# Optimization experiments

Measured on AMD Instinct MI355X. Metric: run time of the kernel, lower is better.

The kernel has to match this reference:

```python
import jax, jax.numpy as jnp
import numpy as np

NUM_HEADS = 16
GROUP_NUM = 4
HIDDEN = 1024
HEAD_DIM = HIDDEN // NUM_HEADS
EPS = 1e-5


def layernorm(x, g, b):
    mu = jnp.mean(x, axis=-1, keepdims=True)
    var = jnp.var(x, axis=-1, keepdims=True)
    return (x - mu) * jax.lax.rsqrt(var + EPS) * g + b


def setup_inputs() -> dict:
    key = jax.random.key(0)
    ks = jax.random.split(key, 12)
    s = 0.02
    return {
        "hidden_state": jax.random.normal(ks[0], (2, 2048, HIDDEN), jnp.float32),
        "wq": jax.random.normal(ks[1], (HIDDEN, HIDDEN), jnp.float32) * s,
        "bq": jnp.zeros((HIDDEN,), jnp.float32),
        "wk": jax.random.normal(ks[2], (GROUP_NUM * HEAD_DIM, HIDDEN), jnp.float32) * s,
        "bk": jnp.zeros((GROUP_NUM * HEAD_DIM,), jnp.float32),
        "wv": jax.random.normal(ks[3], (GROUP_NUM * HEAD_DIM, HIDDEN), jnp.float32) * s,
        "bv": jnp.zeros((GROUP_NUM * HEAD_DIM,), jnp.float32),
        "wo": jax.random.normal(ks[4], (HIDDEN, HIDDEN), jnp.float32) * s,
        "bo": jnp.zeros((HIDDEN,), jnp.float32),
        "ln_g": jnp.ones((HIDDEN,), jnp.float32),
        "ln_b": jnp.zeros((HIDDEN,), jnp.float32),
        "w1": jax.random.normal(ks[5], (HIDDEN, HIDDEN), jnp.float32) * s,
        "b1": jnp.zeros((HIDDEN,), jnp.float32),
        "w2": jax.random.normal(ks[6], (HIDDEN, HIDDEN), jnp.float32) * s,
        "b2": jnp.zeros((HIDDEN,), jnp.float32),
        "fln_g": jnp.ones((HIDDEN,), jnp.float32),
        "fln_b": jnp.zeros((HIDDEN,), jnp.float32),
    }


def reference(hidden_state, wq, bq, wk, bk, wv, bv, wo, bo, ln_g, ln_b,
              w1, b1, w2, b2, fln_g, fln_b):
    B, S, H = hidden_state.shape
    hpg = NUM_HEADS // GROUP_NUM  # heads per KV group

    q = hidden_state @ wq.T + bq  # [B,S,H]
    k = hidden_state @ wk.T + bk  # [B,S,G*D]
    v = hidden_state @ wv.T + bv

    q = q.reshape(B, S, NUM_HEADS, HEAD_DIM).transpose(0, 2, 1, 3)      # [B,Hh,S,D]
    k = k.reshape(B, S, GROUP_NUM, HEAD_DIM).transpose(0, 2, 1, 3)      # [B,G,S,D]
    v = v.reshape(B, S, GROUP_NUM, HEAD_DIM).transpose(0, 2, 1, 3)
    # expand KV groups to full head count (consecutive repeat, matching torch expand+reshape)
    k = jnp.repeat(k, hpg, axis=1)  # [B,Hh,S,D]
    v = jnp.repeat(v, hpg, axis=1)

    scale = 1.0 / jnp.sqrt(jnp.float32(HEAD_DIM))
    scores = jnp.einsum('bhsd,bhtd->bhst', q, k) * scale  # [B,Hh,S,S]
    probs = jax.nn.softmax(scores, axis=-1)
    attn = jnp.einsum('bhst,bhtd->bhsd', probs, v)  # [B,Hh,S,D]

    # Faithful to source: transpose(-1,-2) then raw flat view to [B, S, Hh*D]
    attn = jnp.swapaxes(attn, -1, -2).reshape(B, -1, HEAD_DIM * NUM_HEADS)

    out = layernorm(hidden_state + attn @ wo.T + bo, ln_g, ln_b)
    ffn = out @ w1.T + b1
    ffn = jax.nn.relu(ffn) @ w2.T + b2
    return layernorm(out + ffn, fln_g, fln_b)
```

## Files before the change

### kernel.cpp

```cpp
#include <hip/hip_runtime.h>
#include <math.h>

#define HIDDEN 1024
#define SEQ 2048

typedef __attribute__((ext_vector_type(8))) short short8;
typedef __attribute__((ext_vector_type(4))) float f32x4;

__device__ __forceinline__ unsigned short f2bf(float x) {
  union { float f; unsigned u; } c; c.f = x;
  unsigned r = c.u + 0x7FFFu + ((c.u >> 16) & 1u);
  return (unsigned short)(r >> 16);
}
__device__ __forceinline__ float bf2f(unsigned short h) {
  union { unsigned u; float f; } c; c.u = ((unsigned)h) << 16;
  return c.f;
}

__device__ __forceinline__ void async_copy16(const void* g, void* l) {
  __builtin_amdgcn_global_load_lds(
      (const __attribute__((address_space(1))) unsigned int*)g,
      (__attribute__((address_space(3))) unsigned int*)l, 16, 0, 0);
}

__global__ __launch_bounds__(256) void cvt_all(
    const float* __restrict__ hs, const float* __restrict__ wq,
    const float* __restrict__ wk, const float* __restrict__ wv,
    const float* __restrict__ wo, const float* __restrict__ w1,
    const float* __restrict__ w2,
    unsigned short* __restrict__ hsb, unsigned short* __restrict__ wqb,
    unsigned short* __restrict__ wkb, unsigned short* __restrict__ wvb,
    unsigned short* __restrict__ wob, unsigned short* __restrict__ w1b,
    unsigned short* __restrict__ w2b)
{
  const int i = blockIdx.x * 256 + threadIdx.x;
  const float* src; unsigned short* dst; int off;
  if (i < 1048576)      { src = hs; dst = hsb; off = i; }
  else if (i < 1310720) { src = wq; dst = wqb; off = i - 1048576; }
  else if (i < 1376256) { src = wk; dst = wkb; off = i - 1310720; }
  else if (i < 1441792) { src = wv; dst = wvb; off = i - 1376256; }
  else if (i < 1703936) { src = wo; dst = wob; off = i - 1441792; }
  else if (i < 1966080) { src = w1; dst = w1b; off = i - 1703936; }
  else                  { src = w2; dst = w2b; off = i - 1966080; }
  float4 v = ((const float4*)src)[off];
  ushort4 o;
  o.x = f2bf(v.x); o.y = f2bf(v.y); o.z = f2bf(v.z); o.w = f2bf(v.w);
  ((ushort4*)dst)[off] = o;
}

template<bool RELU>
__global__ __launch_bounds__(256) void gemm_mfma(
    const unsigned short* __restrict__ A, const unsigned short* __restrict__ W,
    const float* __restrict__ bias, unsigned short* __restrict__ C,
    int M, int N, int K)
{
  __shared__ unsigned short As[64 * 64];
  __shared__ unsigned short Bs[64 * 64];
  const int tid = threadIdx.x;
  const int lane = tid & 63, wave = tid >> 6;
  const int ln = lane & 15, quad = lane >> 4;
  const int wm = (wave >> 1) * 32, wn = (wave & 1) * 32;
  const int m0 = blockIdx.y * 64, n0 = blockIdx.x * 64;

  f32x4 acc[2][2];
#pragma unroll
  for (int i = 0; i < 2; ++i)
#pragma unroll
    for (int j = 0; j < 2; ++j) acc[i][j] = (f32x4){0.f, 0.f, 0.f, 0.f};

  for (int k0 = 0; k0 < K; k0 += 64) {
#pragma unroll
    for (int it = 0; it < 2; ++it) {
      const int c = (wave * 2 + it) * 64 + lane;
      const int row = c >> 3, gc = (c & 7) ^ (row & 7);
      async_copy16(A + (size_t)(m0 + row) * K + k0 + gc * 8,
                   &As[(wave * 2 + it) * 512]);
      async_copy16(W + (size_t)(n0 + row) * K + k0 + gc * 8,
                   &Bs[(wave * 2 + it) * 512]);
    }
    __syncthreads();

    short8 af[2][2], bfr[2][2];
#pragma unroll
    for (int i = 0; i < 2; ++i) {
      const int row = wm + i * 16 + ln;
#pragma unroll
      for (int f = 0; f < 2; ++f) {
        const int ch = row * 8 + ((f * 4 + quad) ^ (row & 7));
        af[i][f] = *(const short8*)&As[ch * 8];
      }
    }
#pragma unroll
    for (int j = 0; j < 2; ++j) {
      const int row = wn + j * 16 + ln;
#pragma unroll
      for (int f = 0; f < 2; ++f) {
        const int ch = row * 8 + ((f * 4 + quad) ^ (row & 7));
        bfr[j][f] = *(const short8*)&Bs[ch * 8];
      }
    }
#pragma unroll
    for (int i = 0; i < 2; ++i)
#pragma unroll
      for (int j = 0; j < 2; ++j) {
        acc[i][j] = __builtin_amdgcn_mfma_f32_16x16x32_bf16(af[i][0], bfr[j][0], acc[i][j], 0, 0, 0);
        acc[i][j] = __builtin_amdgcn_mfma_f32_16x16x32_bf16(af[i][1], bfr[j][1], acc[i][j], 0, 0, 0);
      }
    __syncthreads();
  }

#pragma unroll
  for (int j = 0; j < 2; ++j) {
    const int n = n0 + wn + j * 16 + ln;
    const float bv = bias[n];
#pragma unroll
    for (int i = 0; i < 2; ++i) {
#pragma unroll
      for (int rr = 0; rr < 4; ++rr) {
        const int m = m0 + wm + i * 16 + quad * 4 + rr;
        float v = acc[i][j][rr] + bv;
        if (RELU) v = fmaxf(v, 0.f);
        C[(size_t)m * N + n] = f2bf(v);
      }
    }
  }
}

__global__ __launch_bounds__(256) void gemm_qkv(
    const unsigned short* __restrict__ A,
    const unsigned short* __restrict__ Wq, const unsigned short* __restrict__ Wk,
    const unsigned short* __restrict__ Wv,
    const float* __restrict__ bq, const float* __restrict__ bk,
    const float* __restrict__ bv,
    unsigned short* __restrict__ Qo, unsigned short* __restrict__ Ko,
    unsigned short* __restrict__ Vt)
{
  __shared__ unsigned short As[64 * 64];
  __shared__ unsigned short Bs[128 * 64];
  const int bx = blockIdx.x;
  int mode, nw0;
  const unsigned short* W;
  const float* bias;
  if (bx < 8)       { mode = 0; W = Wq; bias = bq; nw0 = bx * 128; }
  else if (bx < 10) { mode = 1; W = Wk; bias = bk; nw0 = (bx - 8) * 128; }
  else              { mode = 2; W = Wv; bias = bv; nw0 = (bx - 10) * 128; }

  const int tid = threadIdx.x;
  const int lane = tid & 63, wave = tid >> 6;
  const int ln = lane & 15, quad = lane >> 4;
  const int wm = (wave >> 1) * 32, wn = (wave & 1) * 64;
  const int m0 = blockIdx.y * 64;
  const int K = 1024;

  f32x4 acc[2][4];
#pragma unroll
  for (int i = 0; i < 2; ++i)
#pragma unroll
    for (int j = 0; j < 4; ++j) acc[i][j] = (f32x4){0.f, 0.f, 0.f, 0.f};

  for (int k0 = 0; k0 < K; k0 += 64) {
#pragma unroll
    for (int it = 0; it < 2; ++it) {
      const int c = (wave * 2 + it) * 64 + lane;
      const int row = c >> 3, gc = (c & 7) ^ (row & 7);
      async_copy16(A + (size_t)(m0 + row) * K + k0 + gc * 8,
                   &As[(wave * 2 + it) * 512]);
    }
#pragma unroll
    for (int it = 0; it < 4; ++it) {
      const int c = (wave * 4 + it) * 64 + lane;
      const int row = c >> 3, gc = (c & 7) ^ (row & 7);
      async_copy16(W + (size_t)(nw0 + row) * K + k0 + gc * 8,
                   &Bs[(wave * 4 + it) * 512]);
    }
    __syncthreads();

    short8 af[2][2], bfr[4][2];
#pragma unroll
    for (int i = 0; i < 2; ++i) {
      const int row = wm + i * 16 + ln;
#pragma unroll
      for (int f = 0; f < 2; ++f) {
        const int ch = row * 8 + ((f * 4 + quad) ^ (row & 7));
        af[i][f] = *(const short8*)&As[ch * 8];
      }
    }
#pragma unroll
    for (int j = 0; j < 4; ++j) {
      const int row = wn + j * 16 + ln;
#pragma unroll
      for (int f = 0; f < 2; ++f) {
        const int ch = row * 8 + ((f * 4 + quad) ^ (row & 7));
        bfr[j][f] = *(const short8*)&Bs[ch * 8];
      }
    }
#pragma unroll
    for (int i = 0; i < 2; ++i)
#pragma unroll
      for (int j = 0; j < 4; ++j) {
        acc[i][j] = __builtin_amdgcn_mfma_f32_16x16x32_bf16(af[i][0], bfr[j][0], acc[i][j], 0, 0, 0);
        acc[i][j] = __builtin_amdgcn_mfma_f32_16x16x32_bf16(af[i][1], bfr[j][1], acc[i][j], 0, 0, 0);
      }
    __syncthreads();
  }

#pragma unroll
  for (int j = 0; j < 4; ++j) {
    const int nl = nw0 + wn + j * 16 + ln;
    const float bvv = bias[nl];
#pragma unroll
    for (int i = 0; i < 2; ++i) {
#pragma unroll
      for (int rr = 0; rr < 4; ++rr) {
        const int m = m0 + wm + i * 16 + quad * 4 + rr;
        const float v = acc[i][j][rr] + bvv;
        if (mode == 0) {
          Qo[(size_t)m * 1024 + nl] = f2bf(v);
        } else if (mode == 1) {
          Ko[(size_t)m * 256 + nl] = f2bf(v);
        } else {
          const int b = m >> 11, s = m & 2047;
          Vt[((size_t)b * 256 + nl) * SEQ + s] = f2bf(v);
        }
      }
    }
  }
}

__global__ __launch_bounds__(256) void attn_mfma(
    const unsigned short* __restrict__ Q, const unsigned short* __restrict__ Kb,
    const unsigned short* __restrict__ Vt, unsigned short* __restrict__ O)
{
  __shared__ unsigned short Ks[2][64 * 64];
  __shared__ unsigned short Vs[2][64 * 64];
  __shared__ unsigned short Ps[4 * 2 * 16 * 64];

  const int bid = blockIdx.x;
  const int qblk = bid & 15, h = (bid >> 4) & 15, b = bid >> 8, g = h >> 2;
  const int tid = threadIdx.x, lane = tid & 63, wave = tid >> 6;
  const int ln = lane & 15, quad = lane >> 4, q8 = quad * 8;
  const int s0 = qblk * 128;
  const float qscale = 0.125f * 1.44269504f;

  const int ln7 = ln & 7;
  const int x0 = (quad ^ ln7) * 8;
  const int x1 = ((4 + quad) ^ ln7) * 8;
  const int pswz = 2 * ln7;
  const int pbase = wave * 2048 + ln * 64;
  int pwr[4], prd[2];
#pragma unroll
  for (int jn = 0; jn < 4; ++jn) pwr[jn] = pbase + (((jn * 4 + quad) ^ pswz) << 2);
#pragma unroll
  for (int F = 0; F < 2; ++F)   prd[F] = pbase + (((8 * F + 2 * quad) ^ pswz) << 2);

  short8 ones;
#pragma unroll
  for (int e = 0; e < 8; ++e) ones[e] = (short)0x3F80;

  short8 qf[2][2];
#pragma unroll
  for (int qg = 0; qg < 2; ++qg) {
    const unsigned short* qsrc =
        Q + ((size_t)(b * SEQ + s0 + wave * 32 + qg * 16 + ln)) * 1024 + h * 64 + q8;
    qf[qg][0] = *(const short8*)qsrc;
    qf[qg][1] = *(const short8*)(qsrc + 32);
#pragma unroll
    for (int e = 0; e < 8; ++e) {
      qf[qg][0][e] = (short)f2bf(bf2f((unsigned short)qf[qg][0][e]) * qscale);
      qf[qg][1][e] = (short)f2bf(bf2f((unsigned short)qf[qg][1][e]) * qscale);
    }
  }

  const int srow = lane >> 3;
  const int sgcc = (lane & 7) ^ srow;

  auto stage = [&](int t0, int p) {
#pragma unroll
    for (int it = 0; it < 2; ++it) {
      const int row = wave * 16 + it * 8 + srow;
      async_copy16(Kb + (size_t)(b * SEQ + t0 + row) * 256 + g * 64 + sgcc * 8,
                   &Ks[p][(wave * 2 + it) * 512]);
      async_copy16(Vt + (size_t)(b * 256 + g * 64 + row) * SEQ + t0 + sgcc * 8,
                   &Vs[p][(wave * 2 + it) * 512]);
    }
  };

  f32x4 of[2][4];
  f32x4 ls[2];
#pragma unroll
  for (int qg = 0; qg < 2; ++qg) {
    ls[qg] = (f32x4){0.f, 0.f, 0.f, 0.f};
#pragma unroll
    for (int jd = 0; jd < 4; ++jd) of[qg][jd] = (f32x4){0.f, 0.f, 0.f, 0.f};
  }

  stage(0, 0);

  for (int t = 0; t < 32; ++t) {
    const int p = t & 1;
    if (t < 31) {
      stage((t + 1) * 64, p ^ 1);
      asm volatile("s_waitcnt vmcnt(4)" ::: "memory");
    } else {
      asm volatile("s_waitcnt vmcnt(0)" ::: "memory");
    }
    __builtin_amdgcn_s_barrier();
    asm volatile("" ::: "memory");

    f32x4 sc[2][4];
#pragma unroll
    for (int jn = 0; jn < 4; ++jn) {
      const int krow = (jn * 16 + ln) * 64;
      const short8 kf0 = *(const short8*)&Ks[p][krow + x0];
      const short8 kf1 = *(const short8*)&Ks[p][krow + x1];
#pragma unroll
      for (int qg = 0; qg < 2; ++qg) {
        f32x4 z = (f32x4){0.f, 0.f, 0.f, 0.f};
        z = __builtin_amdgcn_mfma_f32_16x16x32_bf16(kf0, qf[qg][0], z, 0, 0, 0);
        z = __builtin_amdgcn_mfma_f32_16x16x32_bf16(kf1, qf[qg][1], z, 0, 0, 0);
        sc[qg][jn] = z;
      }
    }

#pragma unroll
    for (int qg = 0; qg < 2; ++qg)
#pragma unroll
      for (int jn = 0; jn < 4; ++jn) {
        union { float f; unsigned u; } c0, c1, c2, c3;
        c0.f = exp2f(sc[qg][jn][0]);
        c1.f = exp2f(sc[qg][jn][1]);
        c2.f = exp2f(sc[qg][jn][2]);
        c3.f = exp2f(sc[qg][jn][3]);
        uint2 pk;
        pk.x = __builtin_amdgcn_perm(c1.u, c0.u, 0x07060302u);
        pk.y = __builtin_amdgcn_perm(c3.u, c2.u, 0x07060302u);
        *(uint2*)&Ps[qg * 1024 + pwr[jn]] = pk;
      }

    short8 pf[2][2];
#pragma unroll
    for (int qg = 0; qg < 2; ++qg) {
      pf[qg][0] = *(const short8*)&Ps[qg * 1024 + prd[0]];
      pf[qg][1] = *(const short8*)&Ps[qg * 1024 + prd[1]];
      ls[qg] = __builtin_amdgcn_mfma_f32_16x16x32_bf16(pf[qg][0], ones, ls[qg], 0, 0, 0);
      ls[qg] = __builtin_amdgcn_mfma_f32_16x16x32_bf16(pf[qg][1], ones, ls[qg], 0, 0, 0);
    }
#pragma unroll
    for (int jd = 0; jd < 4; ++jd) {
      const int vrow = (jd * 16 + ln) * 64;
      const short8 vf0 = *(const short8*)&Vs[p][vrow + x0];
      const short8 vf1 = *(const short8*)&Vs[p][vrow + x1];
#pragma unroll
      for (int qg = 0; qg < 2; ++qg) {
        of[qg][jd] = __builtin_amdgcn_mfma_f32_16x16x32_bf16(pf[qg][0], vf0, of[qg][jd], 0, 0, 0);
        of[qg][jd] = __builtin_amdgcn_mfma_f32_16x16x32_bf16(pf[qg][1], vf1, of[qg][jd], 0, 0, 0);
      }
    }

    asm volatile("" ::: "memory");
    __builtin_amdgcn_s_barrier();
    asm volatile("" ::: "memory");
  }

#pragma unroll
  for (int qg = 0; qg < 2; ++qg) {
    float inv[4];
#pragma unroll
    for (int r = 0; r < 4; ++r) inv[r] = 1.0f / ls[qg][r];
    const int sbase = s0 + wave * 32 + qg * 16 + quad * 4;
#pragma unroll
    for (int jd = 0; jd < 4; ++jd) {
      const int d = jd * 16 + ln;
      ushort4 ov;
      ov.x = f2bf(of[qg][jd][0] * inv[0]);
      ov.y = f2bf(of[qg][jd][1] * inv[1]);
      ov.z = f2bf(of[qg][jd][2] * inv[2]);
      ov.w = f2bf(of[qg][jd][3] * inv[3]);
      *(ushort4*)&O[((size_t)b * 1024 + h * 64 + d) * SEQ + sbase] = ov;
    }
  }
}

__device__ __forceinline__ void ln_core(float x[4], const float* gam, const float* bet,
                                        int tid, float out[4]) {
  float s1 = x[0] + x[1] + x[2] + x[3];
  float s2 = x[0] * x[0] + x[1] * x[1] + x[2] * x[2] + x[3] * x[3];
#pragma unroll
  for (int off = 1; off < 64; off <<= 1) {
    s1 += __shfl_xor(s1, off);
    s2 += __shfl_xor(s2, off);
  }
  __shared__ float r1[4], r2[4];
  const int wave = tid >> 6;
  if ((tid & 63) == 0) { r1[wave] = s1; r2[wave] = s2; }
  __syncthreads();
  s1 = r1[0] + r1[1] + r1[2] + r1[3];
  s2 = r2[0] + r2[1] + r2[2] + r2[3];
  const float mu  = s1 * (1.0f / HIDDEN);
  const float var = s2 * (1.0f / HIDDEN) - mu * mu;
  const float inv = rsqrtf(var + 1e-5f);
  float4 gv = *(const float4*)&gam[tid * 4];
  float4 bv = *(const float4*)&bet[tid * 4];
  out[0] = (x[0] - mu) * inv * gv.x + bv.x;
  out[1] = (x[1] - mu) * inv * gv.y + bv.y;
  out[2] = (x[2] - mu) * inv * gv.z + bv.z;
  out[3] = (x[3] - mu) * inv * gv.w + bv.w;
}

__global__ __launch_bounds__(256) void resid_ln1(
    const float* __restrict__ X, const unsigned short* __restrict__ Y,
    const float* __restrict__ gam, const float* __restrict__ bet,
    unsigned short* __restrict__ outb)
{
  const int row = blockIdx.x, tid = threadIdx.x;
  const size_t base = (size_t)row * HIDDEN + tid * 4;
  float4 a = *(const float4*)&X[base];
  ushort4 yv = *(const ushort4*)&Y[base];
  float x[4] = {a.x + bf2f(yv.x), a.y + bf2f(yv.y), a.z + bf2f(yv.z), a.w + bf2f(yv.w)};
  float o[4];
  ln_core(x, gam, bet, tid, o);
  ushort4 ov;
  ov.x = f2bf(o[0]); ov.y = f2bf(o[1]); ov.z = f2bf(o[2]); ov.w = f2bf(o[3]);
  *(ushort4*)&outb[base] = ov;
}

__global__ __launch_bounds__(256) void resid_ln2(
    const unsigned short* __restrict__ X, const unsigned short* __restrict__ Y,
    const float* __restrict__ gam, const float* __restrict__ bet,
    float* __restrict__ out)
{
  const int row = blockIdx.x, tid = threadIdx.x;
  const size_t base = (size_t)row * HIDDEN + tid * 4;
  ushort4 xv = *(const ushort4*)&X[base];
  ushort4 yv = *(const ushort4*)&Y[base];
  float x[4] = {bf2f(xv.x) + bf2f(yv.x), bf2f(xv.y) + bf2f(yv.y),
                bf2f(xv.z) + bf2f(yv.z), bf2f(xv.w) + bf2f(yv.w)};
  float o[4];
  ln_core(x, gam, bet, tid, o);
  float4 ov; ov.x = o[0]; ov.y = o[1]; ov.z = o[2]; ov.w = o[3];
  *(float4*)&out[base] = ov;
}

extern "C" void kernel_launch(void* const* d_in, const int* in_sizes, int n_in,
                              void* d_out, int out_size, void* d_ws, size_t ws_size,
                              hipStream_t stream)
{
  (void)in_sizes; (void)n_in; (void)out_size; (void)ws_size;
  const float* hs  = (const float*)d_in[0];
  const float* wq  = (const float*)d_in[1];
  const float* bq  = (const float*)d_in[2];
  const float* wk  = (const float*)d_in[3];
  const float* bk  = (const float*)d_in[4];
  const float* wv  = (const float*)d_in[5];
  const float* bvp = (const float*)d_in[6];
  const float* wo  = (const float*)d_in[7];
  const float* bo  = (const float*)d_in[8];
  const float* lng = (const float*)d_in[9];
  const float* lnb = (const float*)d_in[10];
  const float* w1  = (const float*)d_in[11];
  const float* b1  = (const float*)d_in[12];
  const float* w2  = (const float*)d_in[13];
  const float* b2  = (const float*)d_in[14];
  const float* flg = (const float*)d_in[15];
  const float* flb = (const float*)d_in[16];
  float* out = (float*)d_out;

  unsigned short* w = (unsigned short*)d_ws;
  unsigned short* wqb = w;
  unsigned short* wkb = w + 1048576;
  unsigned short* wvb = w + 1310720;
  unsigned short* wob = w + 1572864;
  unsigned short* w1b = w + 2621440;
  unsigned short* w2b = w + 3670016;
  unsigned short* hsb = w + 4718592;
  unsigned short* qb  = w + 8912896;
  unsigned short* kb  = w + 13107200;
  unsigned short* vt  = w + 14155776;
  unsigned short* att = w + 15204352;
  unsigned short* f1b = hsb;
  unsigned short* yb  = qb;
  unsigned short* obb = att;
  unsigned short* f2b = qb;

  dim3 blk(256);
  cvt_all<<<dim3(8704), blk, 0, stream>>>(hs, wq, wk, wv, wo, w1, w2,
                                          hsb, wqb, wkb, wvb, wob, w1b, w2b);

  gemm_qkv<<<dim3(12, 64), blk, 0, stream>>>(hsb, wqb, wkb, wvb, bq, bk, bvp,
                                             qb, kb, vt);
  attn_mfma<<<dim3(512), blk, 0, stream>>>(qb, kb, vt, att);
  gemm_mfma<false><<<dim3(16, 64), blk, 0, stream>>>(att, wob, bo, yb, 4096, 1024, 1024);
  resid_ln1<<<dim3(4096), blk, 0, stream>>>(hs, yb, lng, lnb, obb);
  gemm_mfma<true><<<dim3(16, 64), blk, 0, stream>>>(obb, w1b, b1, f1b, 4096, 1024, 1024);
  gemm_mfma<false><<<dim3(16, 64), blk, 0, stream>>>(f1b, w2b, b2, f2b, 4096, 1024, 1024);
  resid_ln2<<<dim3(4096), blk, 0, stream>>>(obb, f2b, flg, flb, out);
}
```

Baseline: 254.9 us.

## Double-buffer wider GEMM tiles and keep attention probabilities in registers

Result: faster. 242.4 us (-4.9%).

```diff
diff --git a/kernel.cpp b/kernel.cpp
--- a/kernel.cpp
+++ b/kernel.cpp
@@ -15,6 +15,20 @@
 __device__ __forceinline__ float bf2f(unsigned short h) {
   union { unsigned u; float f; } c; c.u = ((unsigned)h) << 16;
   return c.f;
+}
+
+__device__ __forceinline__ float fexp2(float x) {
+#if __has_builtin(__builtin_amdgcn_exp2f)
+  return __builtin_amdgcn_exp2f(x);
+#else
+  float r; asm("v_exp_f32 %0, %1" : "=v"(r) : "v"(x)); return r;
+#endif
+}
+
+__device__ __forceinline__ unsigned cvt_pk_bf16(float lo, float hi) {
+  unsigned r;
+  asm("v_cvt_pk_bf16_f32 %0, %1, %2" : "=v"(r) : "v"(lo), "v"(hi));
+  return r;
 }
 
 __device__ __forceinline__ void async_copy16(const void* g, void* l) {
@@ -49,68 +63,89 @@
 }
 
 template<bool RELU>
-__global__ __launch_bounds__(256) void gemm_mfma(
+__global__ __launch_bounds__(256) void gemm_wide(
     const unsigned short* __restrict__ A, const unsigned short* __restrict__ W,
     const float* __restrict__ bias, unsigned short* __restrict__ C,
     int M, int N, int K)
 {
-  __shared__ unsigned short As[64 * 64];
-  __shared__ unsigned short Bs[64 * 64];
+  __shared__ unsigned short As[2][64 * 64];
+  __shared__ unsigned short Bs[2][128 * 64];
   const int tid = threadIdx.x;
   const int lane = tid & 63, wave = tid >> 6;
   const int ln = lane & 15, quad = lane >> 4;
-  const int wm = (wave >> 1) * 32, wn = (wave & 1) * 32;
-  const int m0 = blockIdx.y * 64, n0 = blockIdx.x * 64;
-
-  f32x4 acc[2][2];
+  const int wm = (wave >> 1) * 32, wn = (wave & 1) * 64;
+  const int m0 = blockIdx.y * 64, n0 = blockIdx.x * 128;
+
+  f32x4 acc[2][4];
 #pragma unroll
   for (int i = 0; i < 2; ++i)
 #pragma unroll
-    for (int j = 0; j < 2; ++j) acc[i][j] = (f32x4){0.f, 0.f, 0.f, 0.f};
-
-  for (int k0 = 0; k0 < K; k0 += 64) {
+    for (int j = 0; j < 4; ++j) acc[i][j] = (f32x4){0.f, 0.f, 0.f, 0.f};
+
+  auto stage = [&](int k0, int p) {
 #pragma unroll
     for (int it = 0; it < 2; ++it) {
       const int c = (wave * 2 + it) * 64 + lane;
       const int row = c >> 3, gc = (c & 7) ^ (row & 7);
       async_copy16(A + (size_t)(m0 + row) * K + k0 + gc * 8,
-                   &As[(wave * 2 + it) * 512]);
+                   &As[p][(wave * 2 + it) * 512]);
+    }
+#pragma unroll
+    for (int it = 0; it < 4; ++it) {
+      const int c = (wave * 4 + it) * 64 + lane;
+      const int row = c >> 3, gc = (c & 7) ^ (row & 7);
       async_copy16(W + (size_t)(n0 + row) * K + k0 + gc * 8,
-                   &Bs[(wave * 2 + it) * 512]);
-    }
-    __syncthreads();
-
-    short8 af[2][2], bfr[2][2];
+                   &Bs[p][(wave * 4 + it) * 512]);
+    }
+  };
+
+  stage(0, 0);
+  const int NT = K >> 6;
+  for (int t = 0; t < NT; ++t) {
+    const int p = t & 1;
+    if (t < NT - 1) {
+      stage((t + 1) * 64, p ^ 1);
+      asm volatile("s_waitcnt vmcnt(6)" ::: "memory");
+    } else {
+      asm volatile("s_waitcnt vmcnt(0)" ::: "memory");
+    }
+    __builtin_amdgcn_s_barrier();
+    asm volatile("" ::: "memory");
+
+    short8 af[2][2], bfr[4][2];
 #pragma unroll
     for (int i = 0; i < 2; ++i) {
       const int row = wm + i * 16 + ln;
 #pragma unroll
       for (int f = 0; f < 2; ++f) {
         const int ch = row * 8 + ((f * 4 + quad) ^ (row & 7));
-        af[i][f] = *(const short8*)&As[ch * 8];
-      }
-    }
-#pragma unroll
-    for (int j = 0; j < 2; ++j) {
+        af[i][f] = *(const short8*)&As[p][ch * 8];
+      }
+    }
+#pragma unroll
+    for (int j = 0; j < 4; ++j) {
       const int row = wn + j * 16 + ln;
 #pragma unroll
       for (int f = 0; f < 2; ++f) {
         const int ch = row * 8 + ((f * 4 + quad) ^ (row & 7));
-        bfr[j][f] = *(const short8*)&Bs[ch * 8];
+        bfr[j][f] = *(const short8*)&Bs[p][ch * 8];
       }
     }
 #pragma unroll
     for (int i = 0; i < 2; ++i)
 #pragma unroll
-      for (int j = 0; j < 2; ++j) {
+      for (int j = 0; j < 4; ++j) {
         acc[i][j] = __builtin_amdgcn_mfma_f32_16x16x32_bf16(af[i][0], bfr[j][0], acc[i][j], 0, 0, 0);
         acc[i][j] = __builtin_amdgcn_mfma_f32_16x16x32_bf16(af[i][1], bfr[j][1], acc[i][j], 0, 0, 0);
       }
-    __syncthreads();
-  }
-
-#pragma unroll
-  for (int j = 0; j < 2; ++j) {
+
+    asm volatile("" ::: "memory");
+    __builtin_amdgcn_s_barrier();
+    asm volatile("" ::: "memory");
+  }
+
+#pragma unroll
+  for (int j = 0; j < 4; ++j) {
     const int n = n0 + wn + j * 16 + ln;
     const float bv = bias[n];
 #pragma unroll
@@ -233,7 +268,6 @@
 {
   __shared__ unsigned short Ks[2][64 * 64];
   __shared__ unsigned short Vs[2][64 * 64];
-  __shared__ unsigned short Ps[4 * 2 * 16 * 64];
 
   const int bid = blockIdx.x;
   const int qblk = bid & 15, h = (bid >> 4) & 15, b = bid >> 8, g = h >> 2;
@@ -245,13 +279,6 @@
   const int ln7 = ln & 7;
   const int x0 = (quad ^ ln7) * 8;
   const int x1 = ((4 + quad) ^ ln7) * 8;
-  const int pswz = 2 * ln7;
-  const int pbase = wave * 2048 + ln * 64;
-  int pwr[4], prd[2];
-#pragma unroll
-  for (int jn = 0; jn < 4; ++jn) pwr[jn] = pbase + (((jn * 4 + quad) ^ pswz) << 2);
-#pragma unroll
-  for (int F = 0; F < 2; ++F)   prd[F] = pbase + (((8 * F + 2 * quad) ^ pswz) << 2);
 
   short8 ones;
 #pragma unroll
@@ -278,7 +305,9 @@
 #pragma unroll
     for (int it = 0; it < 2; ++it) {
       const int row = wave * 16 + it * 8 + srow;
-      async_copy16(Kb + (size_t)(b * SEQ + t0 + row) * 256 + g * 64 + sgcc * 8,
+      const int skey = (row & 32) | ((row & 8) << 1) | ((row & 4) << 1) |
+                       ((row & 16) >> 2) | (row & 3);
+      async_copy16(Kb + (size_t)(b * SEQ + t0 + skey) * 256 + g * 64 + sgcc * 8,
                    &Ks[p][(wave * 2 + it) * 512]);
       async_copy16(Vt + (size_t)(b * 256 + g * 64 + row) * SEQ + t0 + sgcc * 8,
                    &Vs[p][(wave * 2 + it) * 512]);
@@ -322,29 +351,26 @@
       }
     }
 
-#pragma unroll
-    for (int qg = 0; qg < 2; ++qg)
-#pragma unroll
-      for (int jn = 0; jn < 4; ++jn) {
-        union { float f; unsigned u; } c0, c1, c2, c3;
-        c0.f = exp2f(sc[qg][jn][0]);
-        c1.f = exp2f(sc[qg][jn][1]);
-        c2.f = exp2f(sc[qg][jn][2]);
-        c3.f = exp2f(sc[qg][jn][3]);
-        uint2 pk;
-        pk.x = __builtin_amdgcn_perm(c1.u, c0.u, 0x07060302u);
-        pk.y = __builtin_amdgcn_perm(c3.u, c2.u, 0x07060302u);
-        *(uint2*)&Ps[qg * 1024 + pwr[jn]] = pk;
-      }
-
     short8 pf[2][2];
 #pragma unroll
     for (int qg = 0; qg < 2; ++qg) {
-      pf[qg][0] = *(const short8*)&Ps[qg * 1024 + prd[0]];
-      pf[qg][1] = *(const short8*)&Ps[qg * 1024 + prd[1]];
+#pragma unroll
+      for (int jn = 0; jn < 4; ++jn)
+#pragma unroll
+        for (int r = 0; r < 4; ++r) sc[qg][jn][r] = fexp2(sc[qg][jn][r]);
+#pragma unroll
+      for (int F = 0; F < 2; ++F) {
+        union { unsigned u[4]; short8 s; } pk;
+        pk.u[0] = cvt_pk_bf16(sc[qg][2 * F][0], sc[qg][2 * F][1]);
+        pk.u[1] = cvt_pk_bf16(sc[qg][2 * F][2], sc[qg][2 * F][3]);
+        pk.u[2] = cvt_pk_bf16(sc[qg][2 * F + 1][0], sc[qg][2 * F + 1][1]);
+        pk.u[3] = cvt_pk_bf16(sc[qg][2 * F + 1][2], sc[qg][2 * F + 1][3]);
+        pf[qg][F] = pk.s;
+      }
       ls[qg] = __builtin_amdgcn_mfma_f32_16x16x32_bf16(pf[qg][0], ones, ls[qg], 0, 0, 0);
       ls[qg] = __builtin_amdgcn_mfma_f32_16x16x32_bf16(pf[qg][1], ones, ls[qg], 0, 0, 0);
     }
+
 #pragma unroll
     for (int jd = 0; jd < 4; ++jd) {
       const int vrow = (jd * 16 + ln) * 64;
@@ -489,9 +515,9 @@
   gemm_qkv<<<dim3(12, 64), blk, 0, stream>>>(hsb, wqb, wkb, wvb, bq, bk, bvp,
                                              qb, kb, vt);
   attn_mfma<<<dim3(512), blk, 0, stream>>>(qb, kb, vt, att);
-  gemm_mfma<false><<<dim3(16, 64), blk, 0, stream>>>(att, wob, bo, yb, 4096, 1024, 1024);
+  gemm_wide<false><<<dim3(8, 64), blk, 0, stream>>>(att, wob, bo, yb, 4096, 1024, 1024);
   resid_ln1<<<dim3(4096), blk, 0, stream>>>(hs, yb, lng, lnb, obb);
-  gemm_mfma<true><<<dim3(16, 64), blk, 0, stream>>>(obb, w1b, b1, f1b, 4096, 1024, 1024);
-  gemm_mfma<false><<<dim3(16, 64), blk, 0, stream>>>(f1b, w2b, b2, f2b, 4096, 1024, 1024);
+  gemm_wide<true><<<dim3(8, 64), blk, 0, stream>>>(obb, w1b, b1, f1b, 4096, 1024, 1024);
+  gemm_wide<false><<<dim3(8, 64), blk, 0, stream>>>(f1b, w2b, b2, f2b, 4096, 1024, 1024);
   resid_ln2<<<dim3(4096), blk, 0, stream>>>(obb, f2b, flg, flb, out);
 }
```

## Keep attention probabilities in registers, enlarge query tiles, swizzle block order

Applied to the files above, without the earlier changes.

After: 244.1 us. 4.3% less time.

```diff
diff --git a/kernel.cpp b/kernel.cpp
--- a/kernel.cpp
+++ b/kernel.cpp
@@ -15,6 +15,16 @@
 __device__ __forceinline__ float bf2f(unsigned short h) {
   union { unsigned u; float f; } c; c.u = ((unsigned)h) << 16;
   return c.f;
+}
+
+__device__ __forceinline__ float fexp2(float x) {
+  float r; asm("v_exp_f32 %0, %1" : "=v"(r) : "v"(x)); return r;
+}
+
+__device__ __forceinline__ unsigned cvt_pk_bf16(float lo, float hi) {
+  unsigned r;
+  asm("v_cvt_pk_bf16_f32 %0, %1, %2" : "=v"(r) : "v"(lo), "v"(hi));
+  return r;
 }
 
 __device__ __forceinline__ void async_copy16(const void* g, void* l) {
@@ -60,7 +70,11 @@
   const int lane = tid & 63, wave = tid >> 6;
   const int ln = lane & 15, quad = lane >> 4;
   const int wm = (wave >> 1) * 32, wn = (wave & 1) * 32;
-  const int m0 = blockIdx.y * 64, n0 = blockIdx.x * 64;
+
+  const int flat = blockIdx.x;
+  const int swz = (flat & 7) * ((int)gridDim.x >> 3) + (flat >> 3);
+  const int ntx = N >> 6;
+  const int m0 = (swz / ntx) * 64, n0 = (swz % ntx) * 64;
 
   f32x4 acc[2][2];
 #pragma unroll
@@ -137,7 +151,11 @@
 {
   __shared__ unsigned short As[64 * 64];
   __shared__ unsigned short Bs[128 * 64];
-  const int bx = blockIdx.x;
+
+  const int flat = blockIdx.x;
+  const int swz = (flat & 7) * 96 + (flat >> 3);
+  const int bx = swz % 12, by = swz / 12;
+
   int mode, nw0;
   const unsigned short* W;
   const float* bias;
@@ -149,7 +167,7 @@
   const int lane = tid & 63, wave = tid >> 6;
   const int ln = lane & 15, quad = lane >> 4;
   const int wm = (wave >> 1) * 32, wn = (wave & 1) * 64;
-  const int m0 = blockIdx.y * 64;
+  const int m0 = by * 64;
   const int K = 1024;
 
   f32x4 acc[2][4];
@@ -233,35 +251,29 @@
 {
   __shared__ unsigned short Ks[2][64 * 64];
   __shared__ unsigned short Vs[2][64 * 64];
-  __shared__ unsigned short Ps[4 * 2 * 16 * 64];
-
-  const int bid = blockIdx.x;
-  const int qblk = bid & 15, h = (bid >> 4) & 15, b = bid >> 8, g = h >> 2;
+
+  const int hwb = blockIdx.x;
+  const int swz = (hwb & 7) * 32 + (hwb >> 3);
+  const int qblk = swz & 7, h = (swz >> 3) & 15, b = swz >> 7, g = h >> 2;
+
   const int tid = threadIdx.x, lane = tid & 63, wave = tid >> 6;
   const int ln = lane & 15, quad = lane >> 4, q8 = quad * 8;
-  const int s0 = qblk * 128;
+  const int s0 = qblk * 256;
   const float qscale = 0.125f * 1.44269504f;
 
   const int ln7 = ln & 7;
   const int x0 = (quad ^ ln7) * 8;
   const int x1 = ((4 + quad) ^ ln7) * 8;
-  const int pswz = 2 * ln7;
-  const int pbase = wave * 2048 + ln * 64;
-  int pwr[4], prd[2];
-#pragma unroll
-  for (int jn = 0; jn < 4; ++jn) pwr[jn] = pbase + (((jn * 4 + quad) ^ pswz) << 2);
-#pragma unroll
-  for (int F = 0; F < 2; ++F)   prd[F] = pbase + (((8 * F + 2 * quad) ^ pswz) << 2);
 
   short8 ones;
 #pragma unroll
   for (int e = 0; e < 8; ++e) ones[e] = (short)0x3F80;
 
-  short8 qf[2][2];
-#pragma unroll
-  for (int qg = 0; qg < 2; ++qg) {
+  short8 qf[4][2];
+#pragma unroll
+  for (int qg = 0; qg < 4; ++qg) {
     const unsigned short* qsrc =
-        Q + ((size_t)(b * SEQ + s0 + wave * 32 + qg * 16 + ln)) * 1024 + h * 64 + q8;
+        Q + ((size_t)(b * SEQ + s0 + wave * 64 + qg * 16 + ln)) * 1024 + h * 64 + q8;
     qf[qg][0] = *(const short8*)qsrc;
     qf[qg][1] = *(const short8*)(qsrc + 32);
 #pragma unroll
@@ -278,17 +290,19 @@
 #pragma unroll
     for (int it = 0; it < 2; ++it) {
       const int row = wave * 16 + it * 8 + srow;
-      async_copy16(Kb + (size_t)(b * SEQ + t0 + row) * 256 + g * 64 + sgcc * 8,
+      const int skey = (row & 32) | ((row & 8) << 1) | ((row & 4) << 1) |
+                       ((row & 16) >> 2) | (row & 3);
+      async_copy16(Kb + (size_t)(b * SEQ + t0 + skey) * 256 + g * 64 + sgcc * 8,
                    &Ks[p][(wave * 2 + it) * 512]);
       async_copy16(Vt + (size_t)(b * 256 + g * 64 + row) * SEQ + t0 + sgcc * 8,
                    &Vs[p][(wave * 2 + it) * 512]);
     }
   };
 
-  f32x4 of[2][4];
-  f32x4 ls[2];
-#pragma unroll
-  for (int qg = 0; qg < 2; ++qg) {
+  f32x4 of[4][4];
+  f32x4 ls[4];
+#pragma unroll
+  for (int qg = 0; qg < 4; ++qg) {
     ls[qg] = (f32x4){0.f, 0.f, 0.f, 0.f};
 #pragma unroll
     for (int jd = 0; jd < 4; ++jd) of[qg][jd] = (f32x4){0.f, 0.f, 0.f, 0.f};
@@ -307,14 +321,14 @@
     __builtin_amdgcn_s_barrier();
     asm volatile("" ::: "memory");
 
-    f32x4 sc[2][4];
+    f32x4 sc[4][4];
 #pragma unroll
     for (int jn = 0; jn < 4; ++jn) {
       const int krow = (jn * 16 + ln) * 64;
       const short8 kf0 = *(const short8*)&Ks[p][krow + x0];
       const short8 kf1 = *(const short8*)&Ks[p][krow + x1];
 #pragma unroll
-      for (int qg = 0; qg < 2; ++qg) {
+      for (int qg = 0; qg < 4; ++qg) {
         f32x4 z = (f32x4){0.f, 0.f, 0.f, 0.f};
         z = __builtin_amdgcn_mfma_f32_16x16x32_bf16(kf0, qf[qg][0], z, 0, 0, 0);
         z = __builtin_amdgcn_mfma_f32_16x16x32_bf16(kf1, qf[qg][1], z, 0, 0, 0);
@@ -322,36 +336,33 @@
       }
     }
 
-#pragma unroll
-    for (int qg = 0; qg < 2; ++qg)
-#pragma unroll
-      for (int jn = 0; jn < 4; ++jn) {
-        union { float f; unsigned u; } c0, c1, c2, c3;
-        c0.f = exp2f(sc[qg][jn][0]);
-        c1.f = exp2f(sc[qg][jn][1]);
-        c2.f = exp2f(sc[qg][jn][2]);
-        c3.f = exp2f(sc[qg][jn][3]);
-        uint2 pk;
-        pk.x = __builtin_amdgcn_perm(c1.u, c0.u, 0x07060302u);
-        pk.y = __builtin_amdgcn_perm(c3.u, c2.u, 0x07060302u);
-        *(uint2*)&Ps[qg * 1024 + pwr[jn]] = pk;
-      }
-
-    short8 pf[2][2];
-#pragma unroll
-    for (int qg = 0; qg < 2; ++qg) {
-      pf[qg][0] = *(const short8*)&Ps[qg * 1024 + prd[0]];
-      pf[qg][1] = *(const short8*)&Ps[qg * 1024 + prd[1]];
+    short8 pf[4][2];
+#pragma unroll
+    for (int qg = 0; qg < 4; ++qg) {
+#pragma unroll
+      for (int jn = 0; jn < 4; ++jn)
+#pragma unroll
+        for (int r = 0; r < 4; ++r) sc[qg][jn][r] = fexp2(sc[qg][jn][r]);
+#pragma unroll
+      for (int F = 0; F < 2; ++F) {
+        union { unsigned u[4]; short8 s; } pk;
+        pk.u[0] = cvt_pk_bf16(sc[qg][2 * F][0], sc[qg][2 * F][1]);
+        pk.u[1] = cvt_pk_bf16(sc[qg][2 * F][2], sc[qg][2 * F][3]);
+        pk.u[2] = cvt_pk_bf16(sc[qg][2 * F + 1][0], sc[qg][2 * F + 1][1]);
+        pk.u[3] = cvt_pk_bf16(sc[qg][2 * F + 1][2], sc[qg][2 * F + 1][3]);
+        pf[qg][F] = pk.s;
+      }
       ls[qg] = __builtin_amdgcn_mfma_f32_16x16x32_bf16(pf[qg][0], ones, ls[qg], 0, 0, 0);
       ls[qg] = __builtin_amdgcn_mfma_f32_16x16x32_bf16(pf[qg][1], ones, ls[qg], 0, 0, 0);
     }
+
 #pragma unroll
     for (int jd = 0; jd < 4; ++jd) {
       const int vrow = (jd * 16 + ln) * 64;
       const short8 vf0 = *(const short8*)&Vs[p][vrow + x0];
       const short8 vf1 = *(const short8*)&Vs[p][vrow + x1];
 #pragma unroll
-      for (int qg = 0; qg < 2; ++qg) {
+      for (int qg = 0; qg < 4; ++qg) {
         of[qg][jd] = __builtin_amdgcn_mfma_f32_16x16x32_bf16(pf[qg][0], vf0, of[qg][jd], 0, 0, 0);
         of[qg][jd] = __builtin_amdgcn_mfma_f32_16x16x32_bf16(pf[qg][1], vf1, of[qg][jd], 0, 0, 0);
       }
@@ -363,11 +374,11 @@
   }
 
 #pragma unroll
-  for (int qg = 0; qg < 2; ++qg) {
+  for (int qg = 0; qg < 4; ++qg) {
     float inv[4];
 #pragma unroll
     for (int r = 0; r < 4; ++r) inv[r] = 1.0f / ls[qg][r];
-    const int sbase = s0 + wave * 32 + qg * 16 + quad * 4;
+    const int sbase = s0 + wave * 64 + qg * 16 + quad * 4;
 #pragma unroll
     for (int jd = 0; jd < 4; ++jd) {
       const int d = jd * 16 + ln;
@@ -486,12 +497,12 @@
   cvt_all<<<dim3(8704), blk, 0, stream>>>(hs, wq, wk, wv, wo, w1, w2,
                                           hsb, wqb, wkb, wvb, wob, w1b, w2b);
 
-  gemm_qkv<<<dim3(12, 64), blk, 0, stream>>>(hsb, wqb, wkb, wvb, bq, bk, bvp,
-                                             qb, kb, vt);
-  attn_mfma<<<dim3(512), blk, 0, stream>>>(qb, kb, vt, att);
-  gemm_mfma<false><<<dim3(16, 64), blk, 0, stream>>>(att, wob, bo, yb, 4096, 1024, 1024);
+  gemm_qkv<<<dim3(768), blk, 0, stream>>>(hsb, wqb, wkb, wvb, bq, bk, bvp,
+                                          qb, kb, vt);
+  attn_mfma<<<dim3(256), blk, 0, stream>>>(qb, kb, vt, att);
+  gemm_mfma<false><<<dim3(1024), blk, 0, stream>>>(att, wob, bo, yb, 4096, 1024, 1024);
   resid_ln1<<<dim3(4096), blk, 0, stream>>>(hs, yb, lng, lnb, obb);
-  gemm_mfma<true><<<dim3(16, 64), blk, 0, stream>>>(obb, w1b, b1, f1b, 4096, 1024, 1024);
-  gemm_mfma<false><<<dim3(16, 64), blk, 0, stream>>>(f1b, w2b, b2, f2b, 4096, 1024, 1024);
+  gemm_mfma<true><<<dim3(1024), blk, 0, stream>>>(obb, w1b, b1, f1b, 4096, 1024, 1024);
+  gemm_mfma<false><<<dim3(1024), blk, 0, stream>>>(f1b, w2b, b2, f2b, 4096, 1024, 1024);
   resid_ln2<<<dim3(4096), blk, 0, stream>>>(obb, f2b, flg, flb, out);
 }
```
